# Kernel optimization log

Measured on AMD Instinct MI355X. Metric: run time of the kernel, lower is better.

The kernel has to match this reference:

```python
import jax, jax.numpy as jnp
import numpy as np

NUDGE = 1e-7

def _norm(x):
    # global mean + L2-norm over axes (1,2), per sample (faithful to source)
    size = x.shape[1] * x.shape[2]
    mean = jnp.sum(x, axis=(1, 2), keepdims=True) / size
    xc = x - mean
    l2 = jnp.sqrt(jnp.sum(xc * xc, axis=(1, 2), keepdims=True))
    return xc / (l2 + NUDGE)


def setup_inputs() -> dict:
    key = jax.random.key(0)
    ks = jax.random.split(key, 9)
    B, D, S, F = 8, 512, 4096, 2048
    s = 0.02
    x = jax.random.normal(ks[0], (B, D, S), dtype=jnp.float32)
    Wq = jax.random.normal(ks[1], (D, D), dtype=jnp.float32) * s
    Wk = jax.random.normal(ks[2], (D, D), dtype=jnp.float32) * s
    Wv = jax.random.normal(ks[3], (D, D), dtype=jnp.float32) * s
    Wo = jax.random.normal(ks[4], (D, D), dtype=jnp.float32) * s
    W1 = jax.random.normal(ks[5], (D, F), dtype=jnp.float32) * s
    b1 = jnp.zeros((F,), dtype=jnp.float32)
    W2 = jax.random.normal(ks[6], (F, D), dtype=jnp.float32) * s
    b2 = jnp.zeros((D,), dtype=jnp.float32)
    return {"x": x, "Wq": Wq, "Wk": Wk, "Wv": Wv, "Wo": Wo,
            "W1": W1, "b1": b1, "W2": W2, "b2": b2}


def reference(x, Wq, Wk, Wv, Wo, W1, b1, W2, b2):
    B, D, S = x.shape
    xt = jnp.swapaxes(x, 1, 2)                      # [B,S,D]
    q = xt @ Wq                                     # [B,S,D]
    k = xt @ Wk
    v = xt @ Wv
    scores = jnp.einsum('bsd,btd->bst', q, k) / jnp.sqrt(jnp.float32(D))
    attn = jax.nn.softmax(scores, axis=-1)          # [B,S,S]
    attn_out = jnp.swapaxes((attn @ v) @ Wo, 1, 2)  # [B,D,S]

    post = _norm(x + attn_out)                      # [B,D,S]

    # per-slice feedforward+linear loop == batched matmul over token axis
    pt = jnp.swapaxes(post, 1, 2)                   # [B,S,D]
    h = jax.nn.relu(pt @ W1 + b1) @ W2 + b2         # [B,S,D]
    return _norm(post + jnp.swapaxes(h, 1, 2))
```

## Files before the change

### kernel.cpp

```cpp
#include <hip/hip_runtime.h>


typedef unsigned short u16;
typedef __attribute__((ext_vector_type(4))) float f32x4;
typedef __attribute__((ext_vector_type(8))) short s16x8;

__device__ __forceinline__ float bf2f(u16 u) {
    unsigned int v = ((unsigned int)u) << 16;
    float f;
    __builtin_memcpy(&f, &v, 4);
    return f;
}
__device__ __forceinline__ u16 f2bf(float f) {
    unsigned int v;
    __builtin_memcpy(&v, &f, 4);
    unsigned int r = (v + 0x7fffu + ((v >> 16) & 1u)) >> 16;
    return (u16)r;
}
__device__ __forceinline__ u16 loadbf(const void* p, long long i, int f32) {
    return f32 ? f2bf(((const float*)p)[i]) : ((const u16*)p)[i];
}

#if defined(__has_builtin)
#if __has_builtin(__builtin_amdgcn_global_load_lds)
#define HAS_GLDS 1
#endif
#endif
#ifndef HAS_GLDS
#define HAS_GLDS 0
#endif

#if HAS_GLDS
__device__ __forceinline__ void glds16(const u16* g, u16* l) {
    __builtin_amdgcn_global_load_lds(
        (const __attribute__((address_space(1))) void*)g,
        (__attribute__((address_space(3))) void*)l, 16, 0, 0);
}
#else
__device__ __forceinline__ void glds16(const u16* g, u16* l) {
    *(int4*)l = *(const int4*)g;
}
#endif

struct DetectArgs { const u16* p[9]; int n[9]; };

__global__ __launch_bounds__(256) void detect9(DetectArgs a, int* __restrict__ flags)
{
    const u16* p = a.p[blockIdx.x];
    const int n_u16 = a.n[blockIdx.x];
    int insane = 0;
    for (int i = threadIdx.x; i < n_u16; i += 256) {
        u16 h = p[i];
        int e = (h >> 7) & 0xFF;
        int m = h & 0x7F;
        bool sane = (e >= 96 && e <= 141) || (e == 0 && m == 0);
        insane += sane ? 0 : 1;
    }
#pragma unroll
    for (int off = 32; off > 0; off >>= 1) insane += __shfl_down(insane, off);
    __shared__ int red[4];
    if ((threadIdx.x & 63) == 0) red[threadIdx.x >> 6] = insane;
    __syncthreads();
    if (threadIdx.x == 0)
        flags[blockIdx.x] = (red[0] + red[1] + red[2] + red[3] > n_u16 / 4) ? 1 : 0;
}

#define BM 128
#define BN 128
#define BK 32

template <typename OutT, bool BIAS, bool RELU>
__global__ __launch_bounds__(256) void gemm_bt(
    const u16* __restrict__ A, const u16* __restrict__ Bt, OutT* __restrict__ C,
    const u16* __restrict__ bias, int M, int N, int K,
    int lda, int ldb, int ldc, int wmod,
    long long aZ, long long aW, long long bZ, long long bW, long long cZ,
    int swz)
{
    __shared__ u16 As[2][BM * BK];
    __shared__ u16 Bs[2][BN * BK];

    const int z = blockIdx.z;
    const int g = z / wmod, w = z - g * wmod;
    A  += g * aZ + w * aW;
    Bt += g * bZ + w * bW;
    C  += (long long)z * cZ;

    int bx = blockIdx.x, by = blockIdx.y;
    if (swz) {
        const int gx = gridDim.x;
        int id = by * gx + bx;
        int xcd = id & 7, j = id >> 3;
        bx = j % gx;
        by = (j / gx) * 8 + xcd;
    }

    const int tid = threadIdx.x;
    const int wave = tid >> 6, lane = tid & 63;
    const int wm = wave >> 1, wn = wave & 1;
    const int q = lane >> 4, r = lane & 15;

    const int ar = tid >> 2;
    const int ac = (((tid & 3) ^ ((tid >> 3) & 3)) << 3);
    const int ks = (r >> 1) & 3;

    const u16* Ag = A + (long long)(by * BM + ar) * lda + ac;
    const u16* Bg = Bt + (long long)(bx * BN + ar) * ldb + ac;
    const long long rstepA = 64LL * lda, rstepB = 64LL * ldb;

    f32x4 acc[4][4];
    const f32x4 zero = {0.f, 0.f, 0.f, 0.f};
#pragma unroll
    for (int i = 0; i < 4; ++i)
#pragma unroll
        for (int j = 0; j < 4; ++j) acc[i][j] = zero;

    const int nIter = K / BK;
    glds16(Ag, &As[0][tid * 8]);
    glds16(Ag + rstepA, &As[0][2048 + tid * 8]);
    glds16(Bg, &Bs[0][tid * 8]);
    glds16(Bg + rstepB, &Bs[0][2048 + tid * 8]);
    Ag += BK; Bg += BK;
    __syncthreads();
    for (int it = 0; it < nIter; ++it) {
        const int cur = it & 1, nxt = cur ^ 1;
        if (it + 1 < nIter) {
            glds16(Ag, &As[nxt][tid * 8]);
            glds16(Ag + rstepA, &As[nxt][2048 + tid * 8]);
            glds16(Bg, &Bs[nxt][tid * 8]);
            glds16(Bg + rstepB, &Bs[nxt][2048 + tid * 8]);
            Ag += BK; Bg += BK;
        }
        s16x8 af[4], bf[4];
#pragma unroll
        for (int mi = 0; mi < 4; ++mi)
            af[mi] = *(const s16x8*)(&As[cur][(wm * 64 + mi * 16 + r) * BK + ((q ^ ks) << 3)]);
#pragma unroll
        for (int ni = 0; ni < 4; ++ni)
            bf[ni] = *(const s16x8*)(&Bs[cur][(wn * 64 + ni * 16 + r) * BK + ((q ^ ks) << 3)]);
#pragma unroll
        for (int mi = 0; mi < 4; ++mi)
#pragma unroll
            for (int ni = 0; ni < 4; ++ni)
                acc[mi][ni] = __builtin_amdgcn_mfma_f32_16x16x32_bf16(
                    af[mi], bf[ni], acc[mi][ni], 0, 0, 0);
        __syncthreads();
    }

    const int col0 = bx * BN + wn * 64;
    const int row0 = by * BM + wm * 64;
#pragma unroll
    for (int ni = 0; ni < 4; ++ni) {
        const int colg = col0 + ni * 16 + r;
        float bv = 0.f;
        if constexpr (BIAS) bv = bf2f(bias[colg]);
#pragma unroll
        for (int mi = 0; mi < 4; ++mi) {
#pragma unroll
            for (int rr = 0; rr < 4; ++rr) {
                const int rowg = row0 + mi * 16 + q * 4 + rr;
                float v = acc[mi][ni][rr] + bv;
                if constexpr (RELU) v = fmaxf(v, 0.f);
                if constexpr (sizeof(OutT) == 2)
                    C[(long long)rowg * ldc + colg] = (OutT)f2bf(v);
                else
                    C[(long long)rowg * ldc + colg] = (OutT)v;
            }
        }
    }
}

template <bool DIRECT>
__global__ __launch_bounds__(1024, 1) void flash_attn(
    const u16* __restrict__ QKV,
    const u16* __restrict__ Vt,
    u16* __restrict__ O,
    float* __restrict__ Opart,
    float* __restrict__ rsPart,
    int nsplit)
{
    __shared__ u16 Qs[64 * 512];
    __shared__ u16 Ks[2][128 * 128];
    __shared__ u16 Ps[64 * 136];
    __shared__ float rsL[16][64];

    const long long SD = 4096LL * 512;
    int g = blockIdx.z, qb = blockIdx.x;
    if (gridDim.z == 8 && gridDim.y == 1) {
        int id = g * 64 + qb;
        g = id & 7; qb = id >> 3;
    }
    const int sp = blockIdx.y;
    const int q0 = qb * 64;
    const u16* Qg = QKV + ((long long)g * 3 + 0) * SD;
    const u16* Kg = QKV + ((long long)g * 3 + 1) * SD;
    const u16* Vg = Vt + (long long)g * SD;

    const int tid = threadIdx.x;
    const int wave = tid >> 6, lane = tid & 63;
    const int q = lane >> 4, r = lane & 15;
    const int mg = wave >> 3, ng = wave & 7;
    const int dg = wave;

#pragma unroll
    for (int i = 0; i < 4; ++i) {
        int L = i * 1024 + tid;
        int row = L >> 6, p = L & 63;
        int l = p ^ (row & 15);
        glds16(Qg + (long long)(q0 + row) * 512 + l * 8, &Qs[L * 8]);
    }

    f32x4 oacc[2][4];
    const f32x4 zero = {0.f, 0.f, 0.f, 0.f};
#pragma unroll
    for (int i = 0; i < 2; ++i)
#pragma unroll
        for (int j = 0; j < 4; ++j) oacc[i][j] = zero;
    float rsum[2][4] = {{0.f, 0.f, 0.f, 0.f}, {0.f, 0.f, 0.f, 0.f}};

    const int span = 4096 / nsplit;
    const int kt0 = sp * span;
    const int ktN = span / 128;
    const float scale = 0.044194173824159216f;

    auto stageK = [&](int ktile, int kc, int buf) {
#pragma unroll
        for (int i = 0; i < 2; ++i) {
            int L = i * 1024 + tid;
            int row = L >> 4, p = L & 15;
            int l = p ^ (row & 15);
            glds16(Kg + (long long)(kt0 + ktile * 128 + row) * 512 + kc * 128 + l * 8,
                   &Ks[buf][L * 8]);
        }
    };
    stageK(0, 0, 0);

    for (int kt = 0; kt < ktN; ++kt) {
        f32x4 sacc[2];
        sacc[0] = zero; sacc[1] = zero;

        for (int kc = 0; kc < 4; ++kc) {
            __syncthreads();
            if (kc < 3) stageK(kt, kc + 1, (kc + 1) & 1);
            const u16* Kb = Ks[kc & 1];
            const int krow = ng * 16 + r;
#pragma unroll
            for (int sc = 0; sc < 4; ++sc) {
                int lk = sc * 4 + q;
                s16x8 bf = *(const s16x8*)&Kb[krow * 128 + ((lk ^ r) << 3)];
#pragma unroll
                for (int mi = 0; mi < 2; ++mi) {
                    int row = mg * 32 + mi * 16 + r;
                    int l = kc * 16 + sc * 4 + q;
                    s16x8 af = *(const s16x8*)&Qs[row * 512 + ((l ^ r) << 3)];
                    sacc[mi] = __builtin_amdgcn_mfma_f32_16x16x32_bf16(
                        af, bf, sacc[mi], 0, 0, 0);
                }
            }
        }
        {
            int col = ng * 16 + r;
#pragma unroll
            for (int mi = 0; mi < 2; ++mi) {
#pragma unroll
                for (int rr = 0; rr < 4; ++rr) {
                    int row = mg * 32 + mi * 16 + q * 4 + rr;
                    float v = __expf(fminf(sacc[mi][rr] * scale, 30.f));
                    Ps[row * 136 + col] = f2bf(v);
                    rsum[mi][rr] += v;
                }
            }
        }
        __syncthreads();
        if (kt + 1 < ktN) stageK(kt + 1, 0, 0);
        const long long vbase = (long long)(dg * 32 + r) * 4096 + kt0 + kt * 128;
#pragma unroll
        for (int kc = 0; kc < 4; ++kc) {
            s16x8 af[2], bf[4];
#pragma unroll
            for (int mi = 0; mi < 2; ++mi)
                af[mi] = *(const s16x8*)(Vg + vbase + (long long)mi * 16 * 4096
                                         + kc * 32 + q * 8);
#pragma unroll
            for (int ni = 0; ni < 4; ++ni)
                bf[ni] = *(const s16x8*)&Ps[(ni * 16 + r) * 136 + kc * 32 + q * 8];
            __builtin_amdgcn_s_setprio(1);
#pragma unroll
            for (int mi = 0; mi < 2; ++mi)
#pragma unroll
                for (int ni = 0; ni < 4; ++ni)
                    oacc[mi][ni] = __builtin_amdgcn_mfma_f32_16x16x32_bf16(
                        af[mi], bf[ni], oacc[mi][ni], 0, 0, 0);
            __builtin_amdgcn_s_setprio(0);
        }
    }

#pragma unroll
    for (int mi = 0; mi < 2; ++mi)
#pragma unroll
        for (int rr = 0; rr < 4; ++rr) {
            float s = rsum[mi][rr];
#pragma unroll
            for (int m = 1; m < 16; m <<= 1) s += __shfl_xor(s, m);
            rsum[mi][rr] = s;
        }
    if (r == 0) {
#pragma unroll
        for (int mi = 0; mi < 2; ++mi)
#pragma unroll
            for (int rr = 0; rr < 4; ++rr)
                rsL[wave][mg * 32 + mi * 16 + q * 4 + rr] = rsum[mi][rr];
    }
    __syncthreads();

    if constexpr (DIRECT) {
        u16* Og = O + (long long)g * SD;
#pragma unroll
        for (int ni = 0; ni < 4; ++ni) {
            int qrow = ni * 16 + r;
            int wb = (qrow >> 5) * 8;
            float rs = 0.f;
#pragma unroll
            for (int j = 0; j < 8; ++j) rs += rsL[wb + j][qrow];
            float inv = 1.f / rs;
#pragma unroll
            for (int mi = 0; mi < 2; ++mi) {
                int d = dg * 32 + mi * 16 + q * 4;
                ushort4 o4;
                o4.x = f2bf(oacc[mi][ni][0] * inv);
                o4.y = f2bf(oacc[mi][ni][1] * inv);
                o4.z = f2bf(oacc[mi][ni][2] * inv);
                o4.w = f2bf(oacc[mi][ni][3] * inv);
                *(ushort4*)&Og[(long long)(q0 + qrow) * 512 + d] = o4;
            }
        }
    } else {
        const int pb = g * nsplit + sp;
        float* Op = Opart + (long long)pb * SD;
#pragma unroll
        for (int ni = 0; ni < 4; ++ni) {
            int qrow = ni * 16 + r;
#pragma unroll
            for (int mi = 0; mi < 2; ++mi) {
                int d = dg * 32 + mi * 16 + q * 4;
                float4 o4;
                o4.x = oacc[mi][ni][0]; o4.y = oacc[mi][ni][1];
                o4.z = oacc[mi][ni][2]; o4.w = oacc[mi][ni][3];
                *(float4*)&Op[(long long)(q0 + qrow) * 512 + d] = o4;
            }
        }
        if (tid < 64) {
            int wb = (tid >> 5) * 8;
            float rs = 0.f;
#pragma unroll
            for (int j = 0; j < 8; ++j) rs += rsL[wb + j][tid];
            rsPart[(long long)pb * 4096 + q0 + tid] = rs;
        }
    }
}

__global__ __launch_bounds__(256) void reduce_flash(
    const float* __restrict__ Opart, const float* __restrict__ rsPart,
    u16* __restrict__ O, int ns)
{
    const long long SD = 4096LL * 512;
    const int g = blockIdx.y;
    u16* Og = O + (long long)g * SD;
    const int base = blockIdx.x * 2048;
#pragma unroll
    for (int it = 0; it < 8; ++it) {
        int i = base + it * 256 + threadIdx.x;
        int row = i >> 9;
        float s = 0.f, rs = 0.f;
        for (int sp = 0; sp < ns; ++sp) {
            s += Opart[(long long)(g * ns + sp) * SD + i];
            rs += rsPart[(long long)(g * ns + sp) * 4096 + row];
        }
        Og[i] = f2bf(s / rs);
    }
}

__global__ __launch_bounds__(256) void transpose_any(
    const void* __restrict__ in, u16* __restrict__ out, int R, int C,
    long long sIn, long long sOut, const int* __restrict__ flag)
{
    __shared__ u16 tile[32][33];
    const int f32 = *flag;
    const long long ib = (long long)blockIdx.z * sIn;
    u16* ob = out + (long long)blockIdx.z * sOut;
    const int c0 = blockIdx.x * 32, r0 = blockIdx.y * 32;
    const int tx = threadIdx.x, ty = threadIdx.y;
#pragma unroll
    for (int i = 0; i < 4; ++i) {
        int rr = ty + i * 8;
        tile[rr][tx] = loadbf(in, ib + (long long)(r0 + rr) * C + c0 + tx, f32);
    }
    __syncthreads();
#pragma unroll
    for (int i = 0; i < 4; ++i) {
        int cc = ty + i * 8;
        ob[(long long)(c0 + cc) * R + r0 + tx] = tile[tx][cc];
    }
}

__global__ __launch_bounds__(256) void transpose_b16(
    const u16* __restrict__ in, u16* __restrict__ out, int R, int C,
    long long sIn, long long sOut)
{
    __shared__ u16 tile[32][33];
    in += (long long)blockIdx.z * sIn;
    out += (long long)blockIdx.z * sOut;
    const int c0 = blockIdx.x * 32, r0 = blockIdx.y * 32;
    const int tx = threadIdx.x, ty = threadIdx.y;
#pragma unroll
    for (int i = 0; i < 4; ++i) {
        int rr = ty + i * 8;
        tile[rr][tx] = in[(long long)(r0 + rr) * C + c0 + tx];
    }
    __syncthreads();
#pragma unroll
    for (int i = 0; i < 4; ++i) {
        int cc = ty + i * 8;
        out[(long long)(c0 + cc) * R + r0 + tx] = tile[tx][cc];
    }
}

__global__ __launch_bounds__(256) void convert_bias(
    const void* __restrict__ b1, const void* __restrict__ b2,
    u16* __restrict__ ob, const int* __restrict__ f1, const int* __restrict__ f2)
{
    int i = blockIdx.x * 256 + threadIdx.x;
    if (i < 2048) ob[i] = loadbf(b1, i, *f1);
    else if (i < 2560) ob[i] = loadbf(b2, i - 2048, *f2);
}

__global__ __launch_bounds__(256) void stats_add_partial(
    const u16* __restrict__ A, const u16* __restrict__ Bv,
    float2* __restrict__ partial)
{
    const int b = blockIdx.y;
    const long long yb = (long long)b * (4096LL * 512);
    const int base = blockIdx.x * 2048;
    float s = 0.f, ss = 0.f;
#pragma unroll
    for (int it = 0; it < 8; ++it) {
        int i = base + it * 256 + threadIdx.x;
        float z = bf2f(A[yb + i]) + bf2f(Bv[yb + i]);
        s += z; ss += z * z;
    }
#pragma unroll
    for (int off = 32; off > 0; off >>= 1) {
        s += __shfl_down(s, off); ss += __shfl_down(ss, off);
    }
    __shared__ float red[8];
    int lane = threadIdx.x & 63, wave = threadIdx.x >> 6;
    if (lane == 0) { red[wave * 2] = s; red[wave * 2 + 1] = ss; }
    __syncthreads();
    if (threadIdx.x == 0) {
        for (int w = 1; w < 4; ++w) { s += red[w * 2]; ss += red[w * 2 + 1]; }
        partial[b * 1024 + blockIdx.x] = make_float2(s, ss);
    }
}

__global__ __launch_bounds__(256) void stats_finish(
    const float2* __restrict__ partial, float2* __restrict__ stats, float N)
{
    const int b = blockIdx.x;
    float s = 0.f, ss = 0.f;
    for (int i = threadIdx.x; i < 1024; i += 256) {
        float2 p = partial[b * 1024 + i];
        s += p.x; ss += p.y;
    }
#pragma unroll
    for (int off = 32; off > 0; off >>= 1) {
        s += __shfl_down(s, off); ss += __shfl_down(ss, off);
    }
    __shared__ float red[8];
    int lane = threadIdx.x & 63, wave = threadIdx.x >> 6;
    if (lane == 0) { red[wave * 2] = s; red[wave * 2 + 1] = ss; }
    __syncthreads();
    if (threadIdx.x == 0) {
        for (int w = 1; w < 4; ++w) { s += red[w * 2]; ss += red[w * 2 + 1]; }
        float mean = s / N;
        float l2 = sqrtf(fmaxf(ss - s * s / N, 0.f));
        stats[b] = make_float2(mean, 1.f / (l2 + 1e-7f));
    }
}

__global__ __launch_bounds__(256) void post_kernel(
    const u16* __restrict__ A, const u16* __restrict__ Bv,
    const float2* __restrict__ stats, u16* __restrict__ post)
{
    const int b = blockIdx.y;
    const float2 st = stats[b];
    const long long yb = (long long)b * (4096LL * 512);
    const int base = blockIdx.x * 2048;
#pragma unroll
    for (int it = 0; it < 8; ++it) {
        int i = base + it * 256 + threadIdx.x;
        float z = bf2f(A[yb + i]) + bf2f(Bv[yb + i]);
        post[yb + i] = f2bf((z - st.x) * st.y);
    }
}

__global__ __launch_bounds__(256) void final_kernel(
    const u16* __restrict__ P, const u16* __restrict__ G,
    const float2* __restrict__ stats, float* __restrict__ out)
{
    __shared__ float tile[32][33];
    const int b = blockIdx.z;
    const float2 st = stats[b];
    const long long bb = (long long)b * (4096LL * 512);
    const int s0 = blockIdx.x * 32, d0 = blockIdx.y * 32;
    const int tx = threadIdx.x, ty = threadIdx.y;
#pragma unroll
    for (int i = 0; i < 4; ++i) {
        int sl = ty + i * 8;
        long long idx = bb + (long long)(s0 + sl) * 512 + d0 + tx;
        tile[sl][tx] = bf2f(P[idx]) + bf2f(G[idx]);
    }
    __syncthreads();
#pragma unroll
    for (int i = 0; i < 4; ++i) {
        int dl = ty + i * 8;
        out[bb + (long long)(d0 + dl) * 4096 + s0 + tx] =
            (tile[tx][dl] - st.x) * st.y;
    }
}

extern "C" void kernel_launch(void* const* d_in, const int* in_sizes, int n_in,
                              void* d_out, int out_size, void* d_ws, size_t ws_size,
                              hipStream_t stream)
{
    (void)out_size;
    const void* x  = d_in[0];
    const void* Wq = d_in[1];
    const void* Wk = d_in[2];
    const void* Wv = d_in[3];
    const void* Wo = d_in[4];
    const void* W1 = d_in[5];
    const void* b1 = d_in[6];
    const void* W2 = d_in[7];
    const void* b2 = d_in[8];

    const int Bb = 8, D = 512, S = 4096, F = 2048;
    const long long SD = (long long)S * D;
    const long long DD = (long long)D * D;

    char* ws = (char*)d_ws;
    size_t off = 0;
    auto take = [&](size_t bytes) -> char* {
        char* p = ws + off;
        off += (bytes + 255) & ~(size_t)255;
        return p;
    };
    u16* xt   = (u16*)take((size_t)Bb * SD * 2);
    u16* WqT  = (u16*)take((size_t)DD * 2);
    u16* WkT  = (u16*)take((size_t)DD * 2);
    u16* WvT  = (u16*)take((size_t)DD * 2);
    u16* WoT  = (u16*)take((size_t)DD * 2);
    u16* W1T  = (u16*)take((size_t)D * F * 2);
    u16* W2T  = (u16*)take((size_t)D * F * 2);
    u16* bb   = (u16*)take(2560 * 2);
    u16* post = (u16*)take((size_t)Bb * SD * 2);
    float2* npart  = (float2*)take(8 * 1024 * sizeof(float2));
    float2* stats1v = (float2*)take(256);
    float2* stats2v = (float2*)take(256);
    int* flags = (int*)take(16 * sizeof(int));
    float* rsPart = (float*)take(4 * 4096 * sizeof(float));

    size_t remaining = ws_size > off ? ws_size - off : 0;
    const size_t perG = (size_t)4 * SD * 2 + 4096;
    int G = (remaining >= 8 * perG) ? 8 : (remaining >= 4 * perG) ? 4 : 2;
    int ns = (G >= 4) ? 1 : 2;

    u16* attnBuf = (u16*)take((size_t)4 * G * SD * 2);
    u16* QKVb = attnBuf;
    u16* Vtb  = attnBuf + (size_t)3 * G * SD;
    float* Opart = (float*)post;
    u16* Oall = (u16*)d_out;
    u16* Y    = post;
    u16* Hbuf = (u16*)d_out;
    u16* Gbuf = attnBuf;

    DetectArgs da;
    for (int i = 0; i < 9; ++i) {
        da.p[i] = (const u16*)d_in[i];
        da.n[i] = (i < n_in && in_sizes[i] < 8192) ? in_sizes[i] : 8192;
    }
    detect9<<<dim3(9), 256, 0, stream>>>(da, flags);

    dim3 tb(32, 8, 1);
    transpose_any<<<dim3(S / 32, D / 32, Bb), tb, 0, stream>>>(x, xt, D, S, SD, SD, flags + 0);
    transpose_any<<<dim3(16, 16, 1), tb, 0, stream>>>(Wq, WqT, D, D, 0, 0, flags + 1);
    transpose_any<<<dim3(16, 16, 1), tb, 0, stream>>>(Wk, WkT, D, D, 0, 0, flags + 2);
    transpose_any<<<dim3(16, 16, 1), tb, 0, stream>>>(Wv, WvT, D, D, 0, 0, flags + 3);
    transpose_any<<<dim3(16, 16, 1), tb, 0, stream>>>(Wo, WoT, D, D, 0, 0, flags + 4);
    transpose_any<<<dim3(F / 32, D / 32, 1), tb, 0, stream>>>(W1, W1T, D, F, 0, 0, flags + 5);
    transpose_any<<<dim3(D / 32, F / 32, 1), tb, 0, stream>>>(W2, W2T, F, D, 0, 0, flags + 7);
    convert_bias<<<10, 256, 0, stream>>>(b1, b2, bb, flags + 6, flags + 8);

    for (int b0 = 0; b0 < Bb; b0 += G) {
        gemm_bt<u16, false, false><<<dim3(D / 128, S / 128, 3 * G), 256, 0, stream>>>(
            xt + (long long)b0 * SD, WqT, QKVb, nullptr, S, D, D, D, D, D,
            3, SD, 0, 0, DD, SD, 1);
        transpose_b16<<<dim3(D / 32, S / 32, G), tb, 0, stream>>>(
            QKVb + 2 * SD, Vtb, S, D, 3 * SD, SD);
        if (ns == 1) {
            flash_attn<true><<<dim3(64, 1, G), 1024, 0, stream>>>(
                QKVb, Vtb, Oall + (long long)b0 * SD, nullptr, nullptr, 1);
        } else {
            flash_attn<false><<<dim3(64, ns, G), 1024, 0, stream>>>(
                QKVb, Vtb, nullptr, Opart, rsPart, ns);
            reduce_flash<<<dim3(1024, G), 256, 0, stream>>>(
                Opart, rsPart, Oall + (long long)b0 * SD, ns);
        }
    }

    gemm_bt<u16, false, false><<<dim3(D / 128, (Bb * S) / 128, 1), 256, 0, stream>>>(
        Oall, WoT, Y, nullptr, Bb * S, D, D, D, D, D, 1, 0, 0, 0, 0, 0, 1);

    stats_add_partial<<<dim3(1024, Bb), 256, 0, stream>>>(xt, Y, npart);
    stats_finish<<<dim3(Bb), 256, 0, stream>>>(npart, stats1v, (float)SD);
    post_kernel<<<dim3(1024, Bb), 256, 0, stream>>>(xt, Y, stats1v, post);

    for (int h = 0; h < 2; ++h) {
        gemm_bt<u16, true, true><<<dim3(F / 128, (4 * S) / 128, 1), 256, 0, stream>>>(
            post + (long long)h * 4 * SD, W1T, Hbuf, bb, 4 * S, F, D, D, D, F,
            1, 0, 0, 0, 0, 0, 1);
        gemm_bt<u16, true, false><<<dim3(D / 128, (4 * S) / 128, 1), 256, 0, stream>>>(
            Hbuf, W2T, Gbuf + (long long)h * 4 * SD, bb + 2048, 4 * S, D, F, F, F, D,
            1, 0, 0, 0, 0, 0, 1);
    }

    stats_add_partial<<<dim3(1024, Bb), 256, 0, stream>>>(post, Gbuf, npart);
    stats_finish<<<dim3(Bb), 256, 0, stream>>>(npart, stats2v, (float)SD);
    final_kernel<<<dim3(S / 32, D / 32, Bb), tb, 0, stream>>>(
        post, Gbuf, stats2v, (float*)d_out);
}
```

Measured before the change: 1.025 ms.

## Add 256x256-tile 8-wave pipelined GEMM for QKV, output and FFN1 projections

Introduces a new GEMM kernel with 256x256 tiles, 512 threads, double-buffered LDS filled by direct global-to-LDS loads, XOR-swizzled layout, and staggered barrier/waitcnt phases that overlap next-tile loads with MFMA work. It replaces the 128x128 gemm_bt for the QKV, Wo and W1 projections to raise data reuse per tile and hide load latency. The larger tiles cut the number of blocks, which may hurt load balance on small grids such as the D=512-wide GEMMs. They also use a large LDS footprint that limits occupancy.

```diff
diff --git a/kernel.cpp b/kernel.cpp
--- a/kernel.cpp
+++ b/kernel.cpp
@@ -41,6 +41,12 @@
     *(int4*)l = *(const int4*)g;
 }
 #endif
+
+#define BARV(N_) do {                                        \
+    asm volatile("s_waitcnt vmcnt(" #N_ ")" ::: "memory");   \
+    __builtin_amdgcn_sched_barrier(0);                       \
+    __builtin_amdgcn_s_barrier();                            \
+    __builtin_amdgcn_sched_barrier(0); } while (0)
 
 struct DetectArgs { const u16* p[9]; int n[9]; };
 
@@ -156,6 +162,141 @@
         if constexpr (BIAS) bv = bf2f(bias[colg]);
 #pragma unroll
         for (int mi = 0; mi < 4; ++mi) {
+#pragma unroll
+            for (int rr = 0; rr < 4; ++rr) {
+                const int rowg = row0 + mi * 16 + q * 4 + rr;
+                float v = acc[mi][ni][rr] + bv;
+                if constexpr (RELU) v = fmaxf(v, 0.f);
+                if constexpr (sizeof(OutT) == 2)
+                    C[(long long)rowg * ldc + colg] = (OutT)f2bf(v);
+                else
+                    C[(long long)rowg * ldc + colg] = (OutT)v;
+            }
+        }
+    }
+}
+
+template <typename OutT, bool BIAS, bool RELU>
+__global__ __attribute__((amdgpu_flat_work_group_size(512, 512)))
+__attribute__((amdgpu_waves_per_eu(2, 2))) void gemm8p(
+    const u16* __restrict__ A, const u16* __restrict__ Bt, OutT* __restrict__ C,
+    const u16* __restrict__ bias, int M, int N, int K,
+    int lda, int ldb, int ldc, int wmod,
+    long long aZ, long long aW, long long bZ, long long bW, long long cZ,
+    int swz)
+{
+    __shared__ u16 As[2][256 * 64];
+    __shared__ u16 Bs[2][256 * 64];
+
+    const int z = blockIdx.z;
+    const int g = z / wmod, w = z - g * wmod;
+    A  += g * aZ + w * aW;
+    Bt += g * bZ + w * bW;
+    C  += (long long)z * cZ;
+
+    int bx = blockIdx.x, by = blockIdx.y;
+    if (swz) {
+        const int gx = gridDim.x;
+        int id = by * gx + bx;
+        int xcd = id & 7, j = id >> 3;
+        bx = j % gx;
+        by = (j / gx) * 8 + xcd;
+    }
+
+    const int tid = threadIdx.x;
+    const int wave = tid >> 6, lane = tid & 63;
+    const int wm = wave >> 2, wn = wave & 3;
+    const int q = lane >> 4, r = lane & 15;
+
+    const u16* Ag = A + (long long)(by * 256) * lda;
+    const u16* Bg = Bt + (long long)(bx * 256) * ldb;
+
+    f32x4 acc[8][4];
+    const f32x4 zero = {0.f, 0.f, 0.f, 0.f};
+#pragma unroll
+    for (int i = 0; i < 8; ++i)
+#pragma unroll
+        for (int j = 0; j < 4; ++j) acc[i][j] = zero;
+
+    auto stA = [&](int T, int piece, int buf) {
+        int row = piece * 64 + (tid >> 3);
+        int cd = tid & 7;
+        glds16(Ag + (long long)row * lda + T * 64 + ((cd ^ (row & 7)) << 3),
+               &As[buf][row * 64 + (cd << 3)]);
+    };
+    auto stB = [&](int T, int piece, int buf) {
+        int row = piece * 64 + (tid >> 3);
+        int cd = tid & 7;
+        glds16(Bg + (long long)row * ldb + T * 64 + ((cd ^ (row & 7)) << 3),
+               &Bs[buf][row * 64 + (cd << 3)]);
+    };
+
+    stB(0, 0, 0); stB(0, 1, 0); stB(0, 2, 0); stB(0, 3, 0);
+    stA(0, 0, 0); stA(0, 2, 0); stA(0, 1, 0); stA(0, 3, 0);
+
+    const int nT = K >> 6;
+    const int rowA0 = wm * 128 + r;
+    const int rowB0 = wn * 64 + r;
+    const int r7 = r & 7;
+
+    for (int T = 0; T < nT; ++T) {
+        const int buf = T & 1, nb = buf ^ 1;
+        const int Tn = (T + 1 < nT) ? T + 1 : 0;
+        const u16* Ab = As[buf];
+        const u16* Bb = Bs[buf];
+        s16x8 bfr[4][2];
+
+#define PH8(QUAD)                                                             \
+        {                                                                     \
+            s16x8 afr[2][2];                                                  \
+            _Pragma("unroll")                                                 \
+            for (int mi = 0; mi < 2; ++mi)                                    \
+                _Pragma("unroll")                                             \
+                for (int t = 0; t < 2; ++t)                                   \
+                    afr[mi][t] = *(const s16x8*)&Ab[(rowA0 + QUAD * 32 + mi * 16) * 64 \
+                                                    + (((t * 4 + q) ^ r7) << 3)];      \
+            __builtin_amdgcn_s_setprio(1);                                    \
+            _Pragma("unroll")                                                 \
+            for (int mi = 0; mi < 2; ++mi)                                    \
+                _Pragma("unroll")                                             \
+                for (int ni = 0; ni < 4; ++ni)                                \
+                    _Pragma("unroll")                                         \
+                    for (int t = 0; t < 2; ++t)                               \
+                        acc[QUAD * 2 + mi][ni] = __builtin_amdgcn_mfma_f32_16x16x32_bf16( \
+                            afr[mi][t], bfr[ni][t], acc[QUAD * 2 + mi][ni], 0, 0, 0);     \
+            __builtin_amdgcn_s_setprio(0);                                    \
+        }
+
+        BARV(2);
+        stB(Tn, 0, nb); stB(Tn, 1, nb);
+#pragma unroll
+        for (int ni = 0; ni < 4; ++ni)
+#pragma unroll
+            for (int t = 0; t < 2; ++t)
+                bfr[ni][t] = *(const s16x8*)&Bb[(rowB0 + ni * 16) * 64
+                                                + (((t * 4 + q) ^ r7) << 3)];
+        PH8(0)
+        BARV(4);
+        stB(Tn, 2, nb); stB(Tn, 3, nb);
+        PH8(1)
+        BARV(4);
+        stA(Tn, 0, nb); stA(Tn, 2, nb);
+        PH8(2)
+        BARV(6);
+        stA(Tn, 1, nb); stA(Tn, 3, nb);
+        PH8(3)
+#undef PH8
+    }
+
+    const int col0 = bx * 256 + wn * 64;
+    const int row0 = by * 256 + wm * 128;
+#pragma unroll
+    for (int ni = 0; ni < 4; ++ni) {
+        const int colg = col0 + ni * 16 + r;
+        float bv = 0.f;
+        if constexpr (BIAS) bv = bf2f(bias[colg]);
+#pragma unroll
+        for (int mi = 0; mi < 8; ++mi) {
 #pragma unroll
             for (int rr = 0; rr < 4; ++rr) {
                 const int rowg = row0 + mi * 16 + q * 4 + rr;
@@ -601,7 +742,7 @@
     convert_bias<<<10, 256, 0, stream>>>(b1, b2, bb, flags + 6, flags + 8);
 
     for (int b0 = 0; b0 < Bb; b0 += G) {
-        gemm_bt<u16, false, false><<<dim3(D / 128, S / 128, 3 * G), 256, 0, stream>>>(
+        gemm8p<u16, false, false><<<dim3(D / 256, S / 256, 3 * G), 512, 0, stream>>>(
             xt + (long long)b0 * SD, WqT, QKVb, nullptr, S, D, D, D, D, D,
             3, SD, 0, 0, DD, SD, 1);
         transpose_b16<<<dim3(D / 32, S / 32, G), tb, 0, stream>>>(
@@ -617,7 +758,7 @@
         }
     }
 
-    gemm_bt<u16, false, false><<<dim3(D / 128, (Bb * S) / 128, 1), 256, 0, stream>>>(
+    gemm8p<u16, false, false><<<dim3(D / 256, (Bb * S) / 256, 1), 512, 0, stream>>>(
         Oall, WoT, Y, nullptr, Bb * S, D, D, D, D, D, 1, 0, 0, 0, 0, 0, 1);
 
     stats_add_partial<<<dim3(1024, Bb), 256, 0, stream>>>(xt, Y, npart);
@@ -625,7 +766,7 @@
     post_kernel<<<dim3(1024, Bb), 256, 0, stream>>>(xt, Y, stats1v, post);
 
     for (int h = 0; h < 2; ++h) {
-        gemm_bt<u16, true, true><<<dim3(F / 128, (4 * S) / 128, 1), 256, 0, stream>>>(
+        gemm8p<u16, true, true><<<dim3(F / 256, (4 * S) / 256, 1), 512, 0, stream>>>(
             post + (long long)h * 4 * SD, W1T, Hbuf, bb, 4 * S, F, D, D, D, F,
             1, 0, 0, 0, 0, 0, 1);
         gemm_bt<u16, true, false><<<dim3(D / 128, (4 * S) / 128, 1), 256, 0, stream>>>(
```

After: 1.111 ms. 1.08x slower.
